# Kernel tuning notes

Hardware: AMD Instinct MI355X
Metric: run time of the kernel (lower is better)

Reference implementation:

```python
import jax, jax.numpy as jnp
import numpy as np
from jax import lax

B = 32
ITERS = 100
ALPHA = 0.3  # keras LeakyReLU default alpha
BN_SCALE = np.float32(1.0 / np.sqrt(1.0 + 1e-3))  # inference BN, default moving stats (mean 0, var 1)


def _make_psf_mat():
    # Gaussian PSF mapping 5184 fine (72x72) code positions -> 81 coarse (9x9) pixels, mat shape (5184, 81)
    sigma = (150.0 / 100.0) * 9.0 / 64.0
    coarse = np.arange(9) + 0.5
    fine = (np.arange(72) + 0.5) * 9.0 / 72.0
    g = np.exp(-(fine[:, None] - coarse[None, :]) ** 2 / (2.0 * sigma ** 2))  # (72, 9)
    mat = np.einsum('ia,jb->ijab', g, g).reshape(5184, 81)
    mat = mat / np.linalg.norm(mat, ord=2)  # spectral-normalize so FISTA (mu=1) is stable
    return mat.astype(np.float32)


def leaky(x):
    return jnp.where(x >= 0, x, ALPHA * x)


def conv(x, k, strides=(1, 1)):
    return lax.conv_general_dilated(x, k, strides, 'SAME',
                                    dimension_numbers=('NHWC', 'HWIO', 'NHWC'))


def _forward(inp, mat, w1_k, w1_b, x1_k, x1_b, c51_k, c51_b, c15_k, c15_b,
             c55_k, c55_b, x2_k, x2_b, y17_k, y17_b, y71_k, y71_b, yc_k, yc_b,
             d1_k, d2_k, h1_w, h1_b, h2_w, h2_b, h3_w, h3_b):
    b = inp.shape[0]
    # w branch
    w = leaky(conv(inp, w1_k) + w1_b)  # (B,9,9,1)
    # z branch -> lambda parameter
    z = inp * BN_SCALE
    z = leaky(conv(z, d1_k, strides=(3, 3)) * BN_SCALE)  # (B,3,3,12), downsample: conv no-bias + BN + LeakyReLU
    z = leaky(conv(z, d2_k, strides=(3, 3)) * BN_SCALE)  # (B,1,1,24)
    z = z.reshape(b, -1)
    z = z @ h1_w + h1_b
    z = z @ h2_w + h2_b
    z = z @ h3_w + h3_b  # (B,1)
    param = 0.1 * jax.nn.sigmoid(z)  # (B,1)
    # x branch: normalize (max of |x| over axis 1 only, as in source)
    x = inp / (0.001 + jnp.max(jnp.abs(inp), axis=1, keepdims=True))
    x = leaky(conv(x, x1_k) + x1_b)  # (B,9,9,3)
    # --- CompressedSensing: 100-iter FISTA, vectorized over batch and 3 channels ---
    im = x.reshape(b, 81, 3).transpose(0, 2, 1)  # (B,3,81) row-major flatten per channel
    lam = (param * 0.1)[:, :, None]  # (B,1,1), mu = 1.0

    def step(carry, _):
        y_tmp, y_last, t = carry
        resid = im - jnp.einsum('bcn,nk->bck', y_tmp, mat)      # (B,3,81)  = im - mat^T y
        re = jnp.einsum('bck,nk->bcn', resid, mat)              # (B,3,5184) = mat (im - mat^T y)
        wv = y_tmp + re
        y_new = jax.nn.relu(wv - lam) - jax.nn.relu(-wv - lam)  # soft threshold
        t_n = (1.0 + jnp.sqrt(1.0 + 4.0 * t * t)) / 2.0
        y_next = y_new + (t - 1.0) / t_n * (y_new - y_last)
        return (y_next, y_new, t_n), None

    init = (jnp.zeros((b, 3, 5184), jnp.float32),
            jnp.zeros((b, 3, 5184), jnp.float32),
            jnp.float32(1.0))
    (_, y_new, _), _ = lax.scan(step, init, None, length=ITERS)
    cs_out = y_new.transpose(0, 2, 1).reshape(b, 72, 72, 3)  # stack channels last then reshape
    x = conv(cs_out, c51_k, strides=(2, 2)) + c51_b   # (B,36,36,16), no activation
    x = conv(x, c15_k, strides=(2, 2)) + c15_b        # (B,18,18,32)
    x = conv(x, c55_k, strides=(2, 2)) + c55_b        # (B,9,9,64)
    x = leaky(conv(x, x2_k) + x2_b)                   # (B,9,9,8)
    # y branch
    y1 = conv(inp, y17_k) + y17_b                     # (B,9,9,32)
    y2 = conv(inp, y71_k) + y71_b                     # (B,9,9,32)
    y = leaky(conv(jnp.concatenate([y1, y2], axis=-1), yc_k) + yc_b)  # (B,9,9,32)
    out = jnp.concatenate([w, x, y], axis=-1)         # (B,9,9,41)
    return out, cs_out


def setup_inputs() -> dict:
    key = jax.random.key(0)
    ks = jax.random.split(key, 20)
    rn = lambda k, s, sc=0.1: sc * jax.random.normal(k, s, dtype=jnp.float32)
    x1_k = jnp.clip(1.0 + 0.3 * jax.random.normal(ks[1], (1, 1, 3, 3)), 0.0, None).astype(jnp.float32)
    return {
        'inp': jax.random.normal(ks[0], (B, 9, 9, 3), dtype=jnp.float32),
        'mat': jnp.asarray(_make_psf_mat()),
        'w1_k': rn(ks[2], (1, 1, 3, 1)), 'w1_b': jnp.zeros((1,), jnp.float32),
        'x1_k': x1_k, 'x1_b': jnp.zeros((3,), jnp.float32),
        'c51_k': rn(ks[3], (5, 1, 3, 16)), 'c51_b': jnp.zeros((16,), jnp.float32),
        'c15_k': rn(ks[4], (1, 5, 16, 32)), 'c15_b': jnp.zeros((32,), jnp.float32),
        'c55_k': rn(ks[5], (5, 5, 32, 64)), 'c55_b': jnp.zeros((64,), jnp.float32),
        'x2_k': rn(ks[6], (1, 1, 64, 8)), 'x2_b': jnp.zeros((8,), jnp.float32),
        'y17_k': rn(ks[7], (1, 7, 3, 32)), 'y17_b': jnp.zeros((32,), jnp.float32),
        'y71_k': rn(ks[8], (7, 1, 3, 32)), 'y71_b': jnp.zeros((32,), jnp.float32),
        'yc_k': rn(ks[9], (1, 1, 64, 32)), 'yc_b': jnp.zeros((32,), jnp.float32),
        'd1_k': rn(ks[10], (5, 5, 3, 12)), 'd2_k': rn(ks[11], (5, 5, 12, 24)),
        'h1_w': rn(ks[12], (24, 24), 0.2), 'h1_b': jnp.zeros((24,), jnp.float32),
        'h2_w': rn(ks[13], (24, 12), 0.2), 'h2_b': jnp.zeros((12,), jnp.float32),
        'h3_w': rn(ks[14], (12, 1), 0.2), 'h3_b': jnp.zeros((1,), jnp.float32),
    }


def reference(inp, mat, w1_k, w1_b, x1_k, x1_b, c51_k, c51_b, c15_k, c15_b,
              c55_k, c55_b, x2_k, x2_b, y17_k, y17_b, y71_k, y71_b, yc_k, yc_b,
              d1_k, d2_k, h1_w, h1_b, h2_w, h2_b, h3_w, h3_b):
    return _forward(inp, mat, w1_k, w1_b, x1_k, x1_b, c51_k, c51_b, c15_k, c15_b,
                    c55_k, c55_b, x2_k, x2_b, y17_k, y17_b, y71_k, y71_b, yc_k, yc_b,
                    d1_k, d2_k, h1_w, h1_b, h2_w, h2_b, h3_w, h3_b)
```

## Files before the change

kernel.cpp:

```cpp
#include <hip/hip_runtime.h>
#include <math.h>

#define LEAKY(x) ((x) >= 0.f ? (x) : 0.3f*(x))

#define G_OFF   0
#define IM_OFF  648
#define LAM_OFF 8424
#define WB_OFF  8456
#define YBR_OFF 11048
#define X1_OFF  93992
#define X2_OFF  757544
#define X3_OFF  1089320

#define OUT0 106272

__global__ __launch_bounds__(256) void prep_kernel(
    const float* __restrict__ inp, const float* __restrict__ mat,
    const float* __restrict__ w1_k, const float* __restrict__ w1_b,
    const float* __restrict__ x1_k, const float* __restrict__ x1_b,
    const float* __restrict__ y17_k, const float* __restrict__ y17_b,
    const float* __restrict__ y71_k, const float* __restrict__ y71_b,
    const float* __restrict__ yc_k, const float* __restrict__ yc_b,
    const float* __restrict__ d1_k, const float* __restrict__ d2_k,
    const float* __restrict__ h1_w, const float* __restrict__ h1_b,
    const float* __restrict__ h2_w, const float* __restrict__ h2_b,
    const float* __restrict__ h3_w, const float* __restrict__ h3_b,
    float* __restrict__ ws)
{
    int t = threadIdx.x;
    if (blockIdx.x == 0) {
        float rs = rsqrtf(mat[0]);
        for (int u = t; u < 648; u += 256) {
            int i = u / 9, a = u % 9;
            ws[G_OFF + u] = mat[(size_t)(i*72)*81 + a*9] * rs;
        }
        return;
    }
    int b = blockIdx.x - 1;
    __shared__ float sin_[243];
    __shared__ float cm[27];
    __shared__ float cat[5184];
    __shared__ float z1[108];
    __shared__ float z2[24];
    __shared__ float v1[24];
    __shared__ float v2[12];

    const float BN  = 1.0f / sqrtf(1.001f);
    const float BN2 = BN * BN;

    for (int u = t; u < 243; u += 256) sin_[u] = inp[b*243 + u];
    __syncthreads();

    if (t < 81) {
        float s = w1_b[0];
        for (int i = 0; i < 3; ++i) s += sin_[t*3+i] * w1_k[i];
        ws[WB_OFF + b*81 + t] = LEAKY(s);
    } else if (t < 108) {
        int u = t - 81;
        float m = 0.f;
        for (int r = 0; r < 9; ++r) m = fmaxf(m, fabsf(sin_[r*27 + u]));
        cm[u] = 0.001f + m;
    }
    if (t >= 128 && t < 236) {
        int u = t - 128;
        int o = u % 12, ox = (u/12) % 3, oy = u/36;
        float s = 0.f;
        for (int kh = 0; kh < 5; ++kh) {
            int iy = oy*3 - 1 + kh;
            if (iy < 0 || iy > 8) continue;
            for (int kw = 0; kw < 5; ++kw) {
                int ix = ox*3 - 1 + kw;
                if (ix < 0 || ix > 8) continue;
                for (int i = 0; i < 3; ++i)
                    s += sin_[(iy*9+ix)*3 + i] * d1_k[((kh*5+kw)*3 + i)*12 + o];
            }
        }
        z1[u] = LEAKY(BN2 * s);
    }
    __syncthreads();

    if (t < 243) {
        int o = t / 81, p = t % 81;
        int c = p % 9;
        float s = x1_b[o];
        for (int i = 0; i < 3; ++i)
            s += (sin_[p*3+i] / cm[c*3+i]) * x1_k[i*3 + o];
        ws[IM_OFF + (b*3 + o)*81 + p] = LEAKY(s);
    }
    __syncthreads();

    if (t < 24) {
        float s = 0.f;
        for (int kh = 1; kh < 4; ++kh)
            for (int kw = 1; kw < 4; ++kw)
                for (int i = 0; i < 12; ++i)
                    s += z1[((kh-1)*3 + (kw-1))*12 + i] * d2_k[((kh*5+kw)*12 + i)*24 + t];
        z2[t] = LEAKY(BN * s);
    }
    __syncthreads();
    if (t < 24) {
        float s = h1_b[t];
        for (int i = 0; i < 24; ++i) s += z2[i] * h1_w[i*24 + t];
        v1[t] = s;
    }
    __syncthreads();
    if (t < 12) {
        float s = h2_b[t];
        for (int i = 0; i < 24; ++i) s += v1[i] * h2_w[i*12 + t];
        v2[t] = s;
    }
    __syncthreads();
    if (t == 0) {
        float s = h3_b[0];
        for (int i = 0; i < 12; ++i) s += v2[i] * h3_w[i];
        ws[LAM_OFF + b] = 0.01f / (1.f + expf(-s));
    }

    for (int u = t; u < 5184; u += 256) {
        int pos = u / 64, i = u % 64;
        int r = pos / 9, c = pos % 9;
        float s;
        if (i < 32) {
            s = y17_b[i];
            for (int kw = 0; kw < 7; ++kw) {
                int cc = c - 3 + kw;
                if (cc < 0 || cc > 8) continue;
                for (int ii = 0; ii < 3; ++ii)
                    s += sin_[(r*9+cc)*3 + ii] * y17_k[(kw*3+ii)*32 + i];
            }
        } else {
            int i2 = i - 32;
            s = y71_b[i2];
            for (int kh = 0; kh < 7; ++kh) {
                int rr = r - 3 + kh;
                if (rr < 0 || rr > 8) continue;
                for (int ii = 0; ii < 3; ++ii)
                    s += sin_[(rr*9+c)*3 + ii] * y71_k[(kh*3+ii)*32 + i2];
            }
        }
        cat[pos*64 + i] = s;
    }
    __syncthreads();
    for (int u = t; u < 2592; u += 256) {
        int pos = u / 32, o = u % 32;
        float s = yc_b[o];
        for (int i = 0; i < 64; ++i) s += cat[pos*64 + i] * yc_k[i*32 + o];
        ws[YBR_OFF + (b*81 + pos)*32 + o] = LEAKY(s);
    }
}

__global__ __launch_bounds__(896, 3) void fista_kernel(
    const float* __restrict__ ws, float* __restrict__ cs_out)
{
    __shared__ float Qt[648];
    __shared__ float U[9*864];
    __shared__ float T[684];
    __shared__ float P[6*84];
    __shared__ float R[108];

    int t = threadIdx.x;
    int b = blockIdx.x / 3, ch = blockIdx.x % 3;
    const float* g = ws + G_OFF;
    float lam = ws[LAM_OFF + b];

    int j = t % 72, grp = t / 72;
    bool act = t < 864;
    bool p13 = t < 648;

    float Gr[54];
    if (act) {
#pragma unroll
        for (int s = 0; s < 6; ++s)
#pragma unroll
            for (int a = 0; a < 9; ++a)
                Gr[s*9 + a] = g[(grp*6 + s)*9 + a];
    }
    float Gj[9];
    if (p13) {
#pragma unroll
        for (int a = 0; a < 9; ++a) Gj[a] = g[j*9 + a];
    }
    int pa = t / 54, prem = t % 54, pb = prem / 6, pseg = prem % 6;
    float GTr[12];
    if (t < 486) {
#pragma unroll
        for (int r = 0; r < 12; ++r) GTr[r] = g[(pseg*12 + r)*9 + pb];
    }
    float im_ab = 0.f;
    if (t < 81) im_ab = ws[IM_OFF + (b*3 + ch)*81 + t];
    if (t < 108) {
        int a = t / 12, c = t % 12;
        R[t] = (c < 9) ? ws[IM_OFF + (b*3 + ch)*81 + a*9 + c] : 0.f;
    }

    float Yv[6], Yl[6];
#pragma unroll
    for (int s = 0; s < 6; ++s) { Yv[s] = 0.f; Yl[s] = 0.f; }
    float tk = 1.f;
    __syncthreads();

    for (int it = 0; it < 100; ++it) {
        if (p13) {
            const float4* R4 = (const float4*)(R + grp*12);
            float4 r0 = R4[0], r1 = R4[1], r2 = R4[2];
            Qt[t] =
                r0.x*Gj[0] + r0.y*Gj[1] + r0.z*Gj[2] + r0.w*Gj[3]
              + r1.x*Gj[4] + r1.y*Gj[5] + r1.z*Gj[6] + r1.w*Gj[7]
              + r2.x*Gj[8];
        }
        __syncthreads();
        float tn = 0.5f*(1.f + sqrtf(1.f + 4.f*tk*tk));
        float cmom = (tk - 1.f) / tn;
        tk = tn;
        if (act) {
            float q0 = Qt[0*72+j], q1 = Qt[1*72+j], q2 = Qt[2*72+j],
                  q3 = Qt[3*72+j], q4 = Qt[4*72+j], q5 = Qt[5*72+j],
                  q6 = Qt[6*72+j], q7 = Qt[7*72+j], q8 = Qt[8*72+j];
            float u0=0,u1=0,u2=0,u3=0,u4=0,u5=0,u6=0,u7=0,u8=0;
#pragma unroll
            for (int s = 0; s < 6; ++s) {
                float re = Gr[s*9+0]*q0 + Gr[s*9+1]*q1 + Gr[s*9+2]*q2
                         + Gr[s*9+3]*q3 + Gr[s*9+4]*q4 + Gr[s*9+5]*q5
                         + Gr[s*9+6]*q6 + Gr[s*9+7]*q7 + Gr[s*9+8]*q8;
                float wv = Yv[s] + re;
                float aa = fabsf(wv) - lam;
                float yn = aa > 0.f ? copysignf(aa, wv) : 0.f;
                float yx = yn + cmom*(yn - Yl[s]);
                Yl[s] = yn; Yv[s] = yx;
                u0 += yx*Gr[s*9+0]; u1 += yx*Gr[s*9+1]; u2 += yx*Gr[s*9+2];
                u3 += yx*Gr[s*9+3]; u4 += yx*Gr[s*9+4]; u5 += yx*Gr[s*9+5];
                u6 += yx*Gr[s*9+6]; u7 += yx*Gr[s*9+7]; u8 += yx*Gr[s*9+8];
            }
            U[0*864+t]=u0; U[1*864+t]=u1; U[2*864+t]=u2; U[3*864+t]=u3;
            U[4*864+t]=u4; U[5*864+t]=u5; U[6*864+t]=u6; U[7*864+t]=u7;
            U[8*864+t]=u8;
        }
        if (it == 99) break;
        __syncthreads();
        if (p13) {
            const float* Ua = U + grp*864 + j;
            float s = Ua[0]     + Ua[72]    + Ua[144]   + Ua[216]
                    + Ua[288]   + Ua[360]   + Ua[432]   + Ua[504]
                    + Ua[576]   + Ua[648]   + Ua[720]   + Ua[792];
            T[grp*76 + j] = s;
        }
        __syncthreads();
        if (t < 486) {
            const float4* T4 = (const float4*)(T + pa*76 + pseg*12);
            float4 t0 = T4[0], t1 = T4[1], t2 = T4[2];
            P[pseg*84 + pa*9 + pb] =
                t0.x*GTr[0] + t0.y*GTr[1] + t0.z*GTr[2] + t0.w*GTr[3]
              + t1.x*GTr[4] + t1.y*GTr[5] + t1.z*GTr[6] + t1.w*GTr[7]
              + t2.x*GTr[8] + t2.y*GTr[9] + t2.z*GTr[10]+ t2.w*GTr[11];
        }
        __syncthreads();
        if (t < 81) {
            float s = P[t] + P[84+t] + P[168+t] + P[252+t] + P[336+t] + P[420+t];
            R[(t/9)*12 + (t%9)] = im_ab - s;
        }
        __syncthreads();
    }
    if (act) {
#pragma unroll
        for (int s = 0; s < 6; ++s) {
            int i = grp*6 + s;
            cs_out[(size_t)(b*5184 + i*72 + j)*3 + ch] = Yl[s];
        }
    }
}

__global__ __launch_bounds__(256) void c51_kernel(
    const float* __restrict__ cs, const float* __restrict__ k,
    const float* __restrict__ bias, float* __restrict__ out)
{
    int id = blockIdx.x*256 + threadIdx.x;
    if (id >= 32*36*36*16) return;
    int o = id & 15; int rest = id >> 4;
    int ox = rest % 36; rest /= 36; int oy = rest % 36; int b = rest / 36;
    float s = bias[o];
    int ix = ox*2;
    for (int kh = 0; kh < 5; ++kh) {
        int iy = oy*2 - 1 + kh;
        if (iy < 0 || iy >= 72) continue;
        const float* p = cs + ((size_t)(b*72 + iy)*72 + ix)*3;
        const float* kk = k + kh*48 + o;
        s += p[0]*kk[0] + p[1]*kk[16] + p[2]*kk[32];
    }
    out[id] = s;
}

__global__ __launch_bounds__(256) void c15_kernel(
    const float* __restrict__ x1, const float* __restrict__ k,
    const float* __restrict__ bias, float* __restrict__ out)
{
    int id = blockIdx.x*256 + threadIdx.x;
    if (id >= 32*18*18*32) return;
    int o = id & 31; int rest = id >> 5;
    int ox = rest % 18; rest /= 18; int oy = rest % 18; int b = rest / 18;
    float s = bias[o];
    int iy = oy*2;
    for (int kw = 0; kw < 5; ++kw) {
        int ix = ox*2 - 1 + kw;
        if (ix < 0 || ix >= 36) continue;
        const float* p = x1 + ((size_t)(b*36 + iy)*36 + ix)*16;
        const float* kk = k + kw*512 + o;
        for (int i = 0; i < 16; ++i) s += p[i]*kk[i*32];
    }
    out[id] = s;
}

__global__ __launch_bounds__(256) void c55_kernel(
    const float* __restrict__ x2, const float* __restrict__ k,
    const float* __restrict__ bias, float* __restrict__ out)
{
    int id = blockIdx.x*256 + threadIdx.x;
    if (id >= 32*9*9*64) return;
    int o = id & 63; int rest = id >> 6;
    int ox = rest % 9; rest /= 9; int oy = rest % 9; int b = rest / 9;
    float s = bias[o];
    for (int kh = 0; kh < 5; ++kh) {
        int iy = oy*2 - 1 + kh;
        if (iy < 0 || iy >= 18) continue;
        for (int kw = 0; kw < 5; ++kw) {
            int ix = ox*2 - 1 + kw;
            if (ix < 0 || ix >= 18) continue;
            const float* p = x2 + ((size_t)(b*18 + iy)*18 + ix)*32;
            const float* kk = k + (kh*5+kw)*2048 + o;
            for (int i = 0; i < 32; ++i) s += p[i]*kk[i*64];
        }
    }
    out[id] = s;
}

__global__ __launch_bounds__(256) void out_kernel(
    const float* __restrict__ ws, const float* __restrict__ x2_k,
    const float* __restrict__ x2_b, float* __restrict__ out)
{
    int id = blockIdx.x*256 + threadIdx.x;
    if (id >= OUT0) return;
    int q = id % 41; int rest = id / 41;
    int cc = rest % 9; rest /= 9; int r = rest % 9; int b = rest / 9;
    float val;
    if (q == 0) {
        val = ws[WB_OFF + b*81 + r*9 + cc];
    } else if (q <= 8) {
        int o = q - 1;
        const float* p = ws + X3_OFF + ((size_t)(b*9 + r)*9 + cc)*64;
        float s = x2_b[o];
        for (int i = 0; i < 64; ++i) s += p[i]*x2_k[i*8 + o];
        val = LEAKY(s);
    } else {
        val = ws[YBR_OFF + ((size_t)(b*81 + r*9 + cc))*32 + (q - 9)];
    }
    out[id] = val;
}

extern "C" void kernel_launch(void* const* d_in, const int* in_sizes, int n_in,
                              void* d_out, int out_size, void* d_ws, size_t ws_size,
                              hipStream_t stream) {
    const float* inp   = (const float*)d_in[0];
    const float* mat   = (const float*)d_in[1];
    const float* w1_k  = (const float*)d_in[2];
    const float* w1_b  = (const float*)d_in[3];
    const float* x1_k  = (const float*)d_in[4];
    const float* x1_b  = (const float*)d_in[5];
    const float* c51_k = (const float*)d_in[6];
    const float* c51_b = (const float*)d_in[7];
    const float* c15_k = (const float*)d_in[8];
    const float* c15_b = (const float*)d_in[9];
    const float* c55_k = (const float*)d_in[10];
    const float* c55_b = (const float*)d_in[11];
    const float* x2_k  = (const float*)d_in[12];
    const float* x2_b  = (const float*)d_in[13];
    const float* y17_k = (const float*)d_in[14];
    const float* y17_b = (const float*)d_in[15];
    const float* y71_k = (const float*)d_in[16];
    const float* y71_b = (const float*)d_in[17];
    const float* yc_k  = (const float*)d_in[18];
    const float* yc_b  = (const float*)d_in[19];
    const float* d1_k  = (const float*)d_in[20];
    const float* d2_k  = (const float*)d_in[21];
    const float* h1_w  = (const float*)d_in[22];
    const float* h1_b  = (const float*)d_in[23];
    const float* h2_w  = (const float*)d_in[24];
    const float* h2_b  = (const float*)d_in[25];
    const float* h3_w  = (const float*)d_in[26];
    const float* h3_b  = (const float*)d_in[27];

    float* ws  = (float*)d_ws;
    float* out = (float*)d_out;
    float* cs  = out + OUT0;

    hipLaunchKernelGGL(prep_kernel, dim3(33), dim3(256), 0, stream,
        inp, mat, w1_k, w1_b, x1_k, x1_b, y17_k, y17_b, y71_k, y71_b,
        yc_k, yc_b, d1_k, d2_k, h1_w, h1_b, h2_w, h2_b, h3_w, h3_b, ws);
    hipLaunchKernelGGL(fista_kernel, dim3(96), dim3(896), 0, stream, ws, cs);
    hipLaunchKernelGGL(c51_kernel, dim3(2592), dim3(256), 0, stream, cs, c51_k, c51_b, ws + X1_OFF);
    hipLaunchKernelGGL(c15_kernel, dim3(1296), dim3(256), 0, stream, ws + X1_OFF, c15_k, c15_b, ws + X2_OFF);
    hipLaunchKernelGGL(c55_kernel, dim3(648), dim3(256), 0, stream, ws + X2_OFF, c55_k, c55_b, ws + X3_OFF);
    hipLaunchKernelGGL(out_kernel, dim3(416), dim3(256), 0, stream, ws, x2_k, x2_b, out);
}
```

Before: 402.7 us.

## Restructure FISTA block to use DPP lane reductions and fewer barriers

```diff
diff --git a/kernel.cpp b/kernel.cpp
--- a/kernel.cpp
+++ b/kernel.cpp
@@ -13,6 +13,18 @@
 #define X3_OFF  1089320
 
 #define OUT0 106272
+
+template<int CTRL>
+__device__ __forceinline__ float dpp_add(float v) {
+    int m = __builtin_amdgcn_update_dpp(0, __float_as_int(v), CTRL, 0xF, 0xF, true);
+    return v + __int_as_float(m);
+}
+__device__ __forceinline__ float red8(float v) {
+    v = dpp_add<0xB1>(v);
+    v = dpp_add<0x4E>(v);
+    v = dpp_add<0x141>(v);
+    return v;
+}
 
 __global__ __launch_bounds__(256) void prep_kernel(
     const float* __restrict__ inp, const float* __restrict__ mat,
@@ -149,61 +161,56 @@
     }
 }
 
-__global__ __launch_bounds__(896, 3) void fista_kernel(
+__global__ __launch_bounds__(648, 1) void fista_kernel(
     const float* __restrict__ ws, float* __restrict__ cs_out)
 {
-    __shared__ float Qt[648];
-    __shared__ float U[9*864];
-    __shared__ float T[684];
-    __shared__ float P[6*84];
+    __shared__ float Qtt[864];
+    __shared__ float T[648];
     __shared__ float R[108];
 
     int t = threadIdx.x;
     int b = blockIdx.x / 3, ch = blockIdx.x % 3;
     const float* g = ws + G_OFF;
+    const float* im = ws + IM_OFF + (b*3 + ch)*81;
     float lam = ws[LAM_OFF + b];
 
-    int j = t % 72, grp = t / 72;
-    bool act = t < 864;
-    bool p13 = t < 648;
-
-    float Gr[54];
+    int j1 = t / 9, a1 = t - j1*9;
+    float Gj[9];
+#pragma unroll
+    for (int a = 0; a < 9; ++a) Gj[a] = g[j1*9 + a];
+
+    int j2 = t >> 3, grp = t & 7;
+    bool act = t < 576;
+    float Gr[81];
     if (act) {
 #pragma unroll
-        for (int s = 0; s < 6; ++s)
+        for (int s = 0; s < 9; ++s)
 #pragma unroll
             for (int a = 0; a < 9; ++a)
-                Gr[s*9 + a] = g[(grp*6 + s)*9 + a];
-    }
-    float Gj[9];
-    if (p13) {
-#pragma unroll
-        for (int a = 0; a < 9; ++a) Gj[a] = g[j*9 + a];
-    }
-    int pa = t / 54, prem = t % 54, pb = prem / 6, pseg = prem % 6;
+                Gr[s*9 + a] = g[(grp*9 + s)*9 + a];
+    }
+
+    int ab = t >> 3, seg = t & 7;
+    int a3 = ab / 9, b3 = ab - a3*9;
     float GTr[12];
-    if (t < 486) {
-#pragma unroll
-        for (int r = 0; r < 12; ++r) GTr[r] = g[(pseg*12 + r)*9 + pb];
-    }
-    float im_ab = 0.f;
-    if (t < 81) im_ab = ws[IM_OFF + (b*3 + ch)*81 + t];
-    if (t < 108) {
-        int a = t / 12, c = t % 12;
-        R[t] = (c < 9) ? ws[IM_OFF + (b*3 + ch)*81 + a*9 + c] : 0.f;
-    }
-
-    float Yv[6], Yl[6];
-#pragma unroll
-    for (int s = 0; s < 6; ++s) { Yv[s] = 0.f; Yl[s] = 0.f; }
+#pragma unroll
+    for (int r = 0; r < 12; ++r)
+        GTr[r] = (seg < 6) ? g[(seg*12 + r)*9 + b3] : 0.f;
+    float im_s = (seg == 0) ? im[ab] : 0.f;
+
+    if (t < 81) R[(t/9)*12 + (t%9)] = im[t];
+
+    float Yv[9], Yl[9];
+#pragma unroll
+    for (int s = 0; s < 9; ++s) { Yv[s] = 0.f; Yl[s] = 0.f; }
     float tk = 1.f;
     __syncthreads();
 
     for (int it = 0; it < 100; ++it) {
-        if (p13) {
-            const float4* R4 = (const float4*)(R + grp*12);
+        {
+            const float4* R4 = (const float4*)(R + a1*12);
             float4 r0 = R4[0], r1 = R4[1], r2 = R4[2];
-            Qt[t] =
+            Qtt[j1*12 + a1] =
                 r0.x*Gj[0] + r0.y*Gj[1] + r0.z*Gj[2] + r0.w*Gj[3]
               + r1.x*Gj[4] + r1.y*Gj[5] + r1.z*Gj[6] + r1.w*Gj[7]
               + r2.x*Gj[8];
@@ -212,13 +219,14 @@
         float tn = 0.5f*(1.f + sqrtf(1.f + 4.f*tk*tk));
         float cmom = (tk - 1.f) / tn;
         tk = tn;
+        float u0=0,u1=0,u2=0,u3=0,u4=0,u5=0,u6=0,u7=0,u8=0;
         if (act) {
-            float q0 = Qt[0*72+j], q1 = Qt[1*72+j], q2 = Qt[2*72+j],
-                  q3 = Qt[3*72+j], q4 = Qt[4*72+j], q5 = Qt[5*72+j],
-                  q6 = Qt[6*72+j], q7 = Qt[7*72+j], q8 = Qt[8*72+j];
-            float u0=0,u1=0,u2=0,u3=0,u4=0,u5=0,u6=0,u7=0,u8=0;
-#pragma unroll
-            for (int s = 0; s < 6; ++s) {
+            const float4* Q4 = (const float4*)(Qtt + j2*12);
+            float4 qa = Q4[0], qb = Q4[1], qc = Q4[2];
+            float q0=qa.x,q1=qa.y,q2=qa.z,q3=qa.w,
+                  q4=qb.x,q5=qb.y,q6=qb.z,q7=qb.w,q8=qc.x;
+#pragma unroll
+            for (int s = 0; s < 9; ++s) {
                 float re = Gr[s*9+0]*q0 + Gr[s*9+1]*q1 + Gr[s*9+2]*q2
                          + Gr[s*9+3]*q3 + Gr[s*9+4]*q4 + Gr[s*9+5]*q5
                          + Gr[s*9+6]*q6 + Gr[s*9+7]*q7 + Gr[s*9+8]*q8;
@@ -231,40 +239,37 @@
                 u3 += yx*Gr[s*9+3]; u4 += yx*Gr[s*9+4]; u5 += yx*Gr[s*9+5];
                 u6 += yx*Gr[s*9+6]; u7 += yx*Gr[s*9+7]; u8 += yx*Gr[s*9+8];
             }
-            U[0*864+t]=u0; U[1*864+t]=u1; U[2*864+t]=u2; U[3*864+t]=u3;
-            U[4*864+t]=u4; U[5*864+t]=u5; U[6*864+t]=u6; U[7*864+t]=u7;
-            U[8*864+t]=u8;
         }
         if (it == 99) break;
+        if (act) {
+            u0 = red8(u0); u1 = red8(u1); u2 = red8(u2);
+            u3 = red8(u3); u4 = red8(u4); u5 = red8(u5);
+            u6 = red8(u6); u7 = red8(u7); u8 = red8(u8);
+            float tv = grp==0 ? u0 : grp==1 ? u1 : grp==2 ? u2 : grp==3 ? u3
+                     : grp==4 ? u4 : grp==5 ? u5 : grp==6 ? u6 : u7;
+            T[grp*72 + j2] = tv;
+            if (grp == 0) T[8*72 + j2] = u8;
+        }
         __syncthreads();
-        if (p13) {
-            const float* Ua = U + grp*864 + j;
-            float s = Ua[0]     + Ua[72]    + Ua[144]   + Ua[216]
-                    + Ua[288]   + Ua[360]   + Ua[432]   + Ua[504]
-                    + Ua[576]   + Ua[648]   + Ua[720]   + Ua[792];
-            T[grp*76 + j] = s;
+        {
+            float part = 0.f;
+            if (seg < 6) {
+                const float4* T4 = (const float4*)(T + a3*72 + seg*12);
+                float4 t0 = T4[0], t1 = T4[1], t2 = T4[2];
+                part = t0.x*GTr[0] + t0.y*GTr[1] + t0.z*GTr[2] + t0.w*GTr[3]
+                     + t1.x*GTr[4] + t1.y*GTr[5] + t1.z*GTr[6] + t1.w*GTr[7]
+                     + t2.x*GTr[8] + t2.y*GTr[9] + t2.z*GTr[10]+ t2.w*GTr[11];
+            }
+            part = red8(part);
+            if (seg == 0) R[a3*12 + b3] = im_s - part;
         }
         __syncthreads();
-        if (t < 486) {
-            const float4* T4 = (const float4*)(T + pa*76 + pseg*12);
-            float4 t0 = T4[0], t1 = T4[1], t2 = T4[2];
-            P[pseg*84 + pa*9 + pb] =
-                t0.x*GTr[0] + t0.y*GTr[1] + t0.z*GTr[2] + t0.w*GTr[3]
-              + t1.x*GTr[4] + t1.y*GTr[5] + t1.z*GTr[6] + t1.w*GTr[7]
-              + t2.x*GTr[8] + t2.y*GTr[9] + t2.z*GTr[10]+ t2.w*GTr[11];
-        }
-        __syncthreads();
-        if (t < 81) {
-            float s = P[t] + P[84+t] + P[168+t] + P[252+t] + P[336+t] + P[420+t];
-            R[(t/9)*12 + (t%9)] = im_ab - s;
-        }
-        __syncthreads();
     }
     if (act) {
 #pragma unroll
-        for (int s = 0; s < 6; ++s) {
-            int i = grp*6 + s;
-            cs_out[(size_t)(b*5184 + i*72 + j)*3 + ch] = Yl[s];
+        for (int s = 0; s < 9; ++s) {
+            int i = grp*9 + s;
+            cs_out[(size_t)(b*5184 + i*72 + j2)*3 + ch] = Yl[s];
         }
     }
 }
@@ -394,7 +399,7 @@
     hipLaunchKernelGGL(prep_kernel, dim3(33), dim3(256), 0, stream,
         inp, mat, w1_k, w1_b, x1_k, x1_b, y17_k, y17_b, y71_k, y71_b,
         yc_k, yc_b, d1_k, d2_k, h1_w, h1_b, h2_w, h2_b, h3_w, h3_b, ws);
-    hipLaunchKernelGGL(fista_kernel, dim3(96), dim3(896), 0, stream, ws, cs);
+    hipLaunchKernelGGL(fista_kernel, dim3(96), dim3(648), 0, stream, ws, cs);
     hipLaunchKernelGGL(c51_kernel, dim3(2592), dim3(256), 0, stream, cs, c51_k, c51_b, ws + X1_OFF);
     hipLaunchKernelGGL(c15_kernel, dim3(1296), dim3(256), 0, stream, ws + X1_OFF, c15_k, c15_b, ws + X2_OFF);
     hipLaunchKernelGGL(c55_kernel, dim3(648), dim3(256), 0, stream, ws + X2_OFF, c55_k, c55_b, ws + X3_OFF);
```

Result: slower. 653.6 us (+62.3%).
